# Optimization experiments

Measured on AMD Instinct MI355X. Metric: run time of the kernel, lower is better.

## Reference

```python
import jax, jax.numpy as jnp
import numpy as np
from jax import lax

B, N, C = 32, 512, 512   # N must be 8*8*8 (Convpass reshape)
H, DH = 8, 64            # heads, head_dim
ADIM = 8                 # adapter dim
MLP = 4096
EPS = 1e-5
SCALE = DH ** -0.5


def _ln(x, g, b):
    m = jnp.mean(x, axis=-1, keepdims=True)
    v = jnp.mean((x - m) ** 2, axis=-1, keepdims=True)
    return (x - m) * lax.rsqrt(v + EPS) * g + b


def _qgelu(x):
    return x * jax.nn.sigmoid(1.702 * x)


def _convpass(x, dw, db, cw, cb, uw, ub):
    # x: [B,N,C] -> down [B,N,ADIM]
    d = _qgelu(jnp.einsum('bnc,ca->bna', x, dw) + db)
    p = d.reshape(B, 8, 8, 8, ADIM).transpose(0, 4, 1, 2, 3)  # NCDHW
    p = lax.conv_general_dilated(
        p, cw, window_strides=(1, 1, 1), padding='SAME',
        dimension_numbers=('NCDHW', 'OIDHW', 'NCDHW')) + cb[None, :, None, None, None]
    p = p.transpose(0, 2, 3, 4, 1).reshape(B, N, ADIM)
    return jnp.einsum('bna,ac->bnc', _qgelu(p), uw) + ub


def _attn(x, qkv_w, proj_w, proj_b):
    qkv = jnp.einsum('bnc,ck->bnk', x, qkv_w)            # [B,N,3C]
    qkv = qkv.reshape(B, N, 3, H, DH)
    q, k, v = (qkv[:, :, i].transpose(0, 2, 1, 3) for i in range(3))  # [B,H,N,DH]
    a = jax.nn.softmax(jnp.einsum('bhnd,bhmd->bhnm', q, k) * SCALE, axis=-1)
    o = jnp.einsum('bhnm,bhmd->bhnd', a, v).transpose(0, 2, 1, 3).reshape(B, N, C)
    return jnp.einsum('bnc,ck->bnk', o, proj_w) + proj_b


def setup_inputs() -> dict:
    key = jax.random.key(0)
    ks = jax.random.split(key, 24)
    r = lambda i, shape, s=0.02: jax.random.normal(ks[i], shape, jnp.float32) * s
    inp = {
        'x': jax.random.normal(ks[0], (B, N, C), jnp.float32),
        'pos': jax.random.normal(ks[1], (B, N, C), jnp.float32),
        'ln1_g': jnp.ones((C,), jnp.float32), 'ln1_b': jnp.zeros((C,), jnp.float32),
        'qkv_w': r(2, (C, 3 * C)),
        'proj_w': r(3, (C, C)), 'proj_b': jnp.zeros((C,), jnp.float32),
        'cp1_down_w': r(4, (C, ADIM)), 'cp1_down_b': jnp.zeros((ADIM,), jnp.float32),
        'cp1_conv_w': r(5, (ADIM, ADIM, 3, 3, 3), 0.1), 'cp1_conv_b': jnp.zeros((ADIM,), jnp.float32),
        'cp1_up_w': r(6, (ADIM, C)), 'cp1_up_b': jnp.zeros((C,), jnp.float32),
        'ln2_g': jnp.ones((C,), jnp.float32), 'ln2_b': jnp.zeros((C,), jnp.float32),
        'ff_w1': r(7, (C, MLP)), 'ff_b1': jnp.zeros((MLP,), jnp.float32),
        'ff_w2': r(8, (MLP, C)), 'ff_b2': jnp.zeros((C,), jnp.float32),
        'cp2_down_w': r(9, (C, ADIM)), 'cp2_down_b': jnp.zeros((ADIM,), jnp.float32),
        'cp2_conv_w': r(10, (ADIM, ADIM, 3, 3, 3), 0.1), 'cp2_conv_b': jnp.zeros((ADIM,), jnp.float32),
        'cp2_up_w': r(11, (ADIM, C)), 'cp2_up_b': jnp.zeros((C,), jnp.float32),
    }
    return inp


def reference(x, pos, ln1_g, ln1_b, qkv_w, proj_w, proj_b,
              cp1_down_w, cp1_down_b, cp1_conv_w, cp1_conv_b, cp1_up_w, cp1_up_b,
              ln2_g, ln2_b, ff_w1, ff_b1, ff_w2, ff_b2,
              cp2_down_w, cp2_down_b, cp2_conv_w, cp2_conv_b, cp2_up_w, cp2_up_b):
    x = x + pos
    # attention stage: Residual(PreNormDrop(LN, SelfAttn, Convpass)), dropout=identity (eval)
    h = _ln(x, ln1_g, ln1_b)
    x = x + _attn(h, qkv_w, proj_w, proj_b) + _convpass(h, cp1_down_w, cp1_down_b, cp1_conv_w, cp1_conv_b, cp1_up_w, cp1_up_b)
    # FFN stage: Residual(PreNorm(LN, FFN, Convpass))
    h = _ln(x, ln2_g, ln2_b)
    ffn = jnp.einsum('bnm,mc->bnc', jax.nn.gelu(jnp.einsum('bnc,cm->bnm', h, ff_w1) + ff_b1, approximate=False), ff_w2) + ff_b2
    x = x + ffn + _convpass(h, cp2_down_w, cp2_down_b, cp2_conv_w, cp2_conv_b, cp2_up_w, cp2_up_b)
    return x
```

## Files before the change

kernel.cpp:

```cpp
#include <hip/hip_runtime.h>
#include <math.h>

typedef __bf16 bf16_t;
typedef __bf16 bf16x8 __attribute__((ext_vector_type(8)));
typedef __bf16 bf16x4 __attribute__((ext_vector_type(4)));
typedef float f32x4 __attribute__((ext_vector_type(4)));

constexpr int kB   = 32;
constexpr int kN   = 512;
constexpr int kC   = 512;
constexpr int kH   = 8;
constexpr int kAD  = 8;
constexpr int kMLP = 4096;
constexpr int kBN  = kB * kN;
constexpr float kEPS   = 1e-5f;
constexpr float kSCALE = 0.125f;

__device__ __forceinline__ float qgelu_f(float x) {
    return x / (1.f + __expf(-1.702f * x));
}
__device__ __forceinline__ float gelu_f(float x) {
    float u = 1.5957691216f * x * (1.f + 0.044715f * x * x);
    float e = __expf(u);
    float th = 1.f - 2.f / (e + 1.f);
    return 0.5f * x * (1.f + th);
}

__device__ __forceinline__ unsigned pk2(float a, float b) {
    union { bf16_t h[2]; unsigned u; } z;
    z.h[0] = (bf16_t)a; z.h[1] = (bf16_t)b;
    return z.u;
}

__device__ __forceinline__ void gld_lds16(const void* g, void* l) {
    typedef const __attribute__((address_space(1))) unsigned int* gp_t;
    typedef __attribute__((address_space(3))) unsigned int* lp_t;
    __builtin_amdgcn_global_load_lds((gp_t)(unsigned long long)g,
                                     (lp_t)(unsigned)(unsigned long long)l,
                                     16, 0, 0);
}

__global__ __launch_bounds__(256) void k_addln(
    const float* __restrict__ x, const float* __restrict__ pos,
    const float* __restrict__ g, const float* __restrict__ be,
    float* __restrict__ xout, bf16_t* __restrict__ hout,
    const float* __restrict__ cpv, const float* __restrict__ uwp,
    const float* __restrict__ ubp)
{
    int row = blockIdx.x, tid = threadIdx.x;
    size_t base = (size_t)row * kC;
    __shared__ float s8[8];
    if (cpv) {
        if (tid < 8) s8[tid] = cpv[(size_t)row * 8 + tid];
        __syncthreads();
    }
    float v0 = x[base + tid], v1 = x[base + tid + 256];
    if (pos) { v0 += pos[base + tid]; v1 += pos[base + tid + 256]; }
    if (cpv) {
        float u0 = ubp[tid], u1 = ubp[tid + 256];
        #pragma unroll
        for (int a = 0; a < 8; a++) {
            u0 += s8[a] * uwp[a * kC + tid];
            u1 += s8[a] * uwp[a * kC + tid + 256];
        }
        v0 += u0; v1 += u1;
    }
    if (xout) { xout[base + tid] = v0; xout[base + tid + 256] = v1; }
    float s = v0 + v1, q = v0 * v0 + v1 * v1;
    #pragma unroll
    for (int o = 32; o > 0; o >>= 1) {
        s += __shfl_down(s, o);
        q += __shfl_down(q, o);
    }
    __shared__ float ss[4], sq[4], mrs[2];
    int wv = tid >> 6, ln = tid & 63;
    if (!ln) { ss[wv] = s; sq[wv] = q; }
    __syncthreads();
    if (!tid) {
        float ts = ss[0] + ss[1] + ss[2] + ss[3];
        float tq = sq[0] + sq[1] + sq[2] + sq[3];
        float m = ts * (1.f / kC);
        float var = tq * (1.f / kC) - m * m;
        mrs[0] = m; mrs[1] = rsqrtf(var + kEPS);
    }
    __syncthreads();
    float m = mrs[0], r = mrs[1];
    hout[base + tid]       = (bf16_t)((v0 - m) * r * g[tid] + be[tid]);
    hout[base + tid + 256] = (bf16_t)((v1 - m) * r * g[tid + 256] + be[tid + 256]);
}

__global__ __launch_bounds__(256) void k_transpose_all(
    const float* __restrict__ qkvw, const float* __restrict__ projw,
    const float* __restrict__ fw1,  const float* __restrict__ fw2,
    bf16_t* __restrict__ qkvT, bf16_t* __restrict__ projT,
    bf16_t* __restrict__ fw1T, bf16_t* __restrict__ fw2T)
{
    int id = blockIdx.x;
    const float* w; bf16_t* wt; int K, N, bx, by;
    if (id < 768)       { w = qkvw; wt = qkvT; K = 512;  N = 1536; bx = id % 48;  by = id / 48; }
    else if (id < 1024) { id -= 768;  w = projw; wt = projT; K = 512;  N = 512;  bx = id % 16;  by = id / 16; }
    else if (id < 3072) { id -= 1024; w = fw1;   wt = fw1T;  K = 512;  N = 4096; bx = id % 128; by = id / 128; }
    else                { id -= 3072; w = fw2;   wt = fw2T;  K = 4096; N = 512;  bx = id % 16;  by = id / 16; }
    __shared__ float t[32][33];
    int n0 = bx * 32, k0 = by * 32;
    int tx = threadIdx.x & 31, ty = threadIdx.x >> 5;
    #pragma unroll
    for (int j = 0; j < 32; j += 8)
        t[ty + j][tx] = w[(size_t)(k0 + ty + j) * N + n0 + tx];
    __syncthreads();
    #pragma unroll
    for (int j = 0; j < 32; j += 8)
        wt[(size_t)(n0 + ty + j) * K + k0 + tx] = (bf16_t)t[tx][ty + j];
}

template <int ACT, bool HASB, bool HASR, int OMODE, int K, int LDA, int LDB, int NC>
__global__ __launch_bounds__(256) void k_gemm(
    const bf16_t* __restrict__ A, const bf16_t* __restrict__ Bt,
    const float* __restrict__ bias, const float* __restrict__ res,
    void* __restrict__ outv)
{
    __shared__ bf16_t As[2][128 * 32];
    __shared__ bf16_t Bs[2][128 * 32];
    int tid = threadIdx.x;
    int col0 = blockIdx.x * 128, row0 = blockIdx.y * 128;
    int w = tid >> 6, l = tid & 63;
    int rw0 = (w & 1) * 64, cw0 = (w >> 1) * 64;
    int lr = tid >> 2;
    int lc = (((tid & 3) ^ ((tid >> 3) & 3)) * 8);

    f32x4 acc[4][4];
    #pragma unroll
    for (int i = 0; i < 4; i++)
        #pragma unroll
        for (int j = 0; j < 4; j++)
            acc[i][j] = (f32x4){0.f, 0.f, 0.f, 0.f};

    const bf16_t* Ag  = A  + (size_t)(row0 + lr) * LDA + lc;
    const bf16_t* Ag2 = A  + (size_t)(row0 + 64 + lr) * LDA + lc;
    const bf16_t* Bg  = Bt + (size_t)(col0 + lr) * LDB + lc;
    const bf16_t* Bg2 = Bt + (size_t)(col0 + 64 + lr) * LDB + lc;

    int am = rw0 + (l & 15);
    int bn = cw0 + (l & 15);
    int kq = (l >> 4) * 8;
    int kqA = kq ^ (((am >> 1) & 3) << 3);
    int kqB = kq ^ (((bn >> 1) & 3) << 3);

    for (int k0 = 0; k0 < K; k0 += 64) {
        gld_lds16(Ag + k0, &As[0][tid * 8]);
        gld_lds16(Ag2 + k0, &As[0][2048 + tid * 8]);
        gld_lds16(Bg + k0, &Bs[0][tid * 8]);
        gld_lds16(Bg2 + k0, &Bs[0][2048 + tid * 8]);
        gld_lds16(Ag + k0 + 32, &As[1][tid * 8]);
        gld_lds16(Ag2 + k0 + 32, &As[1][2048 + tid * 8]);
        gld_lds16(Bg + k0 + 32, &Bs[1][tid * 8]);
        gld_lds16(Bg2 + k0 + 32, &Bs[1][2048 + tid * 8]);
        __syncthreads();
        #pragma unroll
        for (int ks = 0; ks < 2; ks++) {
            bf16x8 af[4], bfr[4];
            #pragma unroll
            for (int mt = 0; mt < 4; mt++)
                af[mt] = *(const bf16x8*)&As[ks][(am + mt * 16) * 32 + kqA];
            #pragma unroll
            for (int nt = 0; nt < 4; nt++)
                bfr[nt] = *(const bf16x8*)&Bs[ks][(bn + nt * 16) * 32 + kqB];
            #pragma unroll
            for (int mt = 0; mt < 4; mt++)
                #pragma unroll
                for (int nt = 0; nt < 4; nt++)
                    acc[mt][nt] = __builtin_amdgcn_mfma_f32_16x16x32_bf16(
                        af[mt], bfr[nt], acc[mt][nt], 0, 0, 0);
        }
        __syncthreads();
    }

    #pragma unroll
    for (int mt = 0; mt < 4; mt++) {
        int rowb = row0 + rw0 + mt * 16 + (l >> 4) * 4;
        #pragma unroll
        for (int nt = 0; nt < 4; nt++) {
            int col = col0 + cw0 + nt * 16 + (l & 15);
            float bv = HASB ? bias[col] : 0.f;
            if (OMODE == 2) {
                int which = col >> 9, hd = (col >> 6) & 7, d = col & 63;
                size_t hb = ((size_t)((rowb >> 9) * 8 + hd) * 3 + which) << 15;
                int n0 = rowb & 511;
                if (which == 2) {
                    bf16x4 pk;
                    #pragma unroll
                    for (int p = 0; p < 4; p++) pk[p] = (bf16_t)acc[mt][nt][p];
                    *(bf16x4*)((bf16_t*)outv + hb + (size_t)d * 512 + n0) = pk;
                } else {
                    #pragma unroll
                    for (int p = 0; p < 4; p++)
                        ((bf16_t*)outv)[hb + (size_t)(n0 + p) * 64 + d] =
                            (bf16_t)acc[mt][nt][p];
                }
            } else {
                #pragma unroll
                for (int p = 0; p < 4; p++) {
                    float v = acc[mt][nt][p] + bv;
                    if (ACT == 1) v = qgelu_f(v);
                    if (ACT == 2) v = gelu_f(v);
                    int r = rowb + p;
                    if (OMODE == 0) {
                        if (HASR) v += res[(size_t)r * NC + col];
                        ((float*)outv)[(size_t)r * NC + col] = v;
                    } else {
                        ((bf16_t*)outv)[(size_t)r * NC + col] = (bf16_t)v;
                    }
                }
            }
        }
    }
}

__global__ __launch_bounds__(256) void k_attn(
    const bf16_t* __restrict__ qkvb, bf16_t* __restrict__ obuf)
{
    __shared__ __align__(16) unsigned Ps[4][16 * 36];
    int bid = blockIdx.x;
    int qb = bid & 3, h = (bid >> 2) & 7, b = bid >> 5;
    int t = threadIdx.x, w = t >> 6, l = t & 63;
    const bf16_t* qp  = qkvb + (((size_t)(b * 8 + h) * 3) << 15);
    const bf16_t* kp  = qp + (1 << 15);
    const bf16_t* vtp = qp + (2 << 15);
    int q0 = qb * 128 + w * 32;
    int l15 = l & 15, g = l >> 4, lq = g * 8;
    unsigned* psw = &Ps[w][0];

    bf16x8 aq[2][2];
    #pragma unroll
    for (int mt = 0; mt < 2; mt++)
        #pragma unroll
        for (int kh = 0; kh < 2; kh++) {
            bf16x8 qv = *(const bf16x8*)(qp + (size_t)(q0 + mt * 16 + l15) * 64
                                         + kh * 32 + lq);
            #pragma unroll
            for (int e = 0; e < 8; e++) qv[e] = (bf16_t)((float)qv[e] * kSCALE);
            aq[mt][kh] = qv;
        }

    f32x4 o[2][4];
    float m_run[2], l_run[2];
    #pragma unroll
    for (int mt = 0; mt < 2; mt++) {
        m_run[mt] = -1e30f; l_run[mt] = 0.f;
        #pragma unroll
        for (int dt = 0; dt < 4; dt++) o[mt][dt] = (f32x4){0.f, 0.f, 0.f, 0.f};
    }

    for (int kt = 0; kt < 8; kt++) {
        bf16x8 kf[4][2], vf[4][2];
        #pragma unroll
        for (int nt = 0; nt < 4; nt++)
            #pragma unroll
            for (int kh = 0; kh < 2; kh++)
                kf[nt][kh] = *(const bf16x8*)(kp
                    + (size_t)(kt * 64 + nt * 16 + l15) * 64 + kh * 32 + lq);
        #pragma unroll
        for (int dt = 0; dt < 4; dt++)
            #pragma unroll
            for (int kh = 0; kh < 2; kh++)
                vf[dt][kh] = *(const bf16x8*)(vtp
                    + (size_t)(dt * 16 + l15) * 512 + kt * 64 + kh * 32 + lq);

        #pragma unroll
        for (int mt = 0; mt < 2; mt++) {
            f32x4 sc[4];
            #pragma unroll
            for (int nt = 0; nt < 4; nt++) sc[nt] = (f32x4){0.f, 0.f, 0.f, 0.f};
            #pragma unroll
            for (int nt = 0; nt < 4; nt++)
                #pragma unroll
                for (int kh = 0; kh < 2; kh++)
                    sc[nt] = __builtin_amdgcn_mfma_f32_16x16x32_bf16(
                        kf[nt][kh], aq[mt][kh], sc[nt], 0, 0, 0);
            float mx = sc[0][0];
            #pragma unroll
            for (int nt = 0; nt < 4; nt++)
                #pragma unroll
                for (int p = 0; p < 4; p++) mx = fmaxf(mx, sc[nt][p]);
            mx = fmaxf(mx, __shfl_xor(mx, 16));
            mx = fmaxf(mx, __shfl_xor(mx, 32));
            float mn = fmaxf(m_run[mt], mx);
            float alpha = __expf(m_run[mt] - mn);
            m_run[mt] = mn;
            float rs = 0.f;
            #pragma unroll
            for (int nt = 0; nt < 4; nt++)
                #pragma unroll
                for (int p = 0; p < 4; p++) {
                    float pv = __expf(sc[nt][p] - mn);
                    sc[nt][p] = pv; rs += pv;
                }
            rs += __shfl_xor(rs, 16);
            rs += __shfl_xor(rs, 32);
            l_run[mt] = l_run[mt] * alpha + rs;
            #pragma unroll
            for (int dt = 0; dt < 4; dt++)
                #pragma unroll
                for (int p = 0; p < 4; p++) o[mt][dt][p] *= alpha;
            #pragma unroll
            for (int nt = 0; nt < 4; nt++) {
                uint2 dw;
                dw.x = pk2(sc[nt][0], sc[nt][1]);
                dw.y = pk2(sc[nt][2], sc[nt][3]);
                *(uint2*)&psw[l15 * 36 + nt * 8 + g * 2] = dw;
            }
            asm volatile("" ::: "memory");
            bf16x8 pf0 = *(const bf16x8*)&psw[l15 * 36 + g * 4];
            bf16x8 pf1 = *(const bf16x8*)&psw[l15 * 36 + 16 + g * 4];
            #pragma unroll
            for (int dt = 0; dt < 4; dt++) {
                o[mt][dt] = __builtin_amdgcn_mfma_f32_16x16x32_bf16(
                    vf[dt][0], pf0, o[mt][dt], 0, 0, 0);
                o[mt][dt] = __builtin_amdgcn_mfma_f32_16x16x32_bf16(
                    vf[dt][1], pf1, o[mt][dt], 0, 0, 0);
            }
            asm volatile("" ::: "memory");
        }
    }
    #pragma unroll
    for (int mt = 0; mt < 2; mt++) {
        float inv = 1.f / l_run[mt];
        size_t rbase = ((size_t)b * 512 + q0 + mt * 16 + l15) * 512 + h * 64;
        #pragma unroll
        for (int dt = 0; dt < 4; dt++) {
            bf16x4 pk;
            #pragma unroll
            for (int p = 0; p < 4; p++) pk[p] = (bf16_t)(o[mt][dt][p] * inv);
            *(bf16x4*)&obuf[rbase + dt * 16 + g * 4] = pk;
        }
    }
}

__global__ __launch_bounds__(256) void k_down(
    const bf16_t* __restrict__ h, const float* __restrict__ dw,
    const float* __restrict__ db, float* __restrict__ outp)
{
    __shared__ float sdw[kC * kAD];
    int t = threadIdx.x;
    for (int i = t; i < kC * kAD; i += 256) sdw[i] = dw[i];
    __syncthreads();
    int gt = blockIdx.x * 256 + t;
    int row = gt >> 3, a = gt & 7;
    const bf16x8* hr = (const bf16x8*)(h + (size_t)row * kC);
    float acc = 0.f;
    for (int k8 = 0; k8 < kC / 8; k8++) {
        bf16x8 hv = hr[k8];
        #pragma unroll
        for (int e = 0; e < 8; e++)
            acc += (float)hv[e] * sdw[(k8 * 8 + e) * kAD + a];
    }
    outp[gt] = qgelu_f(acc + db[a]);
}

__global__ __launch_bounds__(512) void k_conv(
    const float* __restrict__ inp, const float* __restrict__ cw,
    const float* __restrict__ cb, float* __restrict__ outp)
{
    __shared__ float si[512 * 9];
    __shared__ float sw[8 * 8 * 27];
    int b = blockIdx.x, t = threadIdx.x;
    for (int i = t; i < 512 * 8; i += 512) {
        int n = i >> 3, a = i & 7;
        si[n * 9 + a] = inp[(size_t)b * 4096 + i];
    }
    for (int i = t; i < 1728; i += 512) sw[i] = cw[i];
    __syncthreads();
    int z = t >> 6, y = (t >> 3) & 7, xx = t & 7;
    float acc[8];
    #pragma unroll
    for (int ao = 0; ao < 8; ao++) acc[ao] = cb[ao];
    for (int dz = -1; dz <= 1; dz++) {
        int zz = z + dz; if ((unsigned)zz > 7u) continue;
        for (int dy = -1; dy <= 1; dy++) {
            int yy = y + dy; if ((unsigned)yy > 7u) continue;
            for (int dx = -1; dx <= 1; dx++) {
                int xn = xx + dx; if ((unsigned)xn > 7u) continue;
                int nn = zz * 64 + yy * 8 + xn;
                int wo = ((dz + 1) * 3 + (dy + 1)) * 3 + (dx + 1);
                #pragma unroll
                for (int ai = 0; ai < 8; ai++) {
                    float iv = si[nn * 9 + ai];
                    #pragma unroll
                    for (int ao = 0; ao < 8; ao++)
                        acc[ao] += iv * sw[(ao * 8 + ai) * 27 + wo];
                }
            }
        }
    }
    #pragma unroll
    for (int ao = 0; ao < 8; ao++)
        outp[(size_t)b * 4096 + t * 8 + ao] = qgelu_f(acc[ao]);
}

__global__ __launch_bounds__(256) void k_up(
    const float* __restrict__ pa, const float* __restrict__ uw,
    const float* __restrict__ ub, float* __restrict__ xbuf)
{
    __shared__ float s[8];
    int row = blockIdx.x, t = threadIdx.x;
    if (t < 8) s[t] = pa[(size_t)row * kAD + t];
    __syncthreads();
    #pragma unroll
    for (int rep = 0; rep < 2; rep++) {
        int c = t + rep * 256;
        float acc = ub[c];
        #pragma unroll
        for (int a = 0; a < 8; a++) acc += s[a] * uw[a * kC + c];
        xbuf[(size_t)row * kC + c] += acc;
    }
}

extern "C" void kernel_launch(void* const* d_in, const int* in_sizes, int n_in,
                              void* d_out, int out_size, void* d_ws, size_t ws_size,
                              hipStream_t stream)
{
    const float* x     = (const float*)d_in[0];
    const float* pos   = (const float*)d_in[1];
    const float* ln1g  = (const float*)d_in[2];
    const float* ln1b  = (const float*)d_in[3];
    const float* qkvw  = (const float*)d_in[4];
    const float* projw = (const float*)d_in[5];
    const float* projb = (const float*)d_in[6];
    const float* dw1   = (const float*)d_in[7];
    const float* db1   = (const float*)d_in[8];
    const float* cw1   = (const float*)d_in[9];
    const float* cb1   = (const float*)d_in[10];
    const float* uw1   = (const float*)d_in[11];
    const float* ub1   = (const float*)d_in[12];
    const float* ln2g  = (const float*)d_in[13];
    const float* ln2b  = (const float*)d_in[14];
    const float* fw1   = (const float*)d_in[15];
    const float* fb1   = (const float*)d_in[16];
    const float* fw2   = (const float*)d_in[17];
    const float* fb2   = (const float*)d_in[18];
    const float* dw2   = (const float*)d_in[19];
    const float* db2   = (const float*)d_in[20];
    const float* cw2   = (const float*)d_in[21];
    const float* cb2   = (const float*)d_in[22];
    const float* uw2   = (const float*)d_in[23];
    const float* ub2   = (const float*)d_in[24];
    float* out = (float*)d_out;

    char* wsb = (char*)d_ws;
    float*  xbuf = (float*)wsb;
    bf16_t* hb   = (bf16_t*)(wsb + 33554432);
    bf16_t* obuf = (bf16_t*)(wsb + 50331648);
    bf16_t* qkvb = (bf16_t*)(wsb + 67108864);
    bf16_t* midb = (bf16_t*)(wsb + 50331648);
    bf16_t* qkvT = (bf16_t*)(wsb + 117440512);
    bf16_t* projT= (bf16_t*)(wsb + 119013376);
    bf16_t* fw1T = (bf16_t*)(wsb + 119537664);
    bf16_t* fw2T = (bf16_t*)(wsb + 123731968);
    float*  cpa  = (float*)(wsb + 127926272);
    float*  cpb  = (float*)(wsb + 128450560);

    k_transpose_all<<<5120, 256, 0, stream>>>(
        qkvw, projw, fw1, fw2, qkvT, projT, fw1T, fw2T);

    k_addln<<<kBN, 256, 0, stream>>>(x, pos, ln1g, ln1b, xbuf, hb,
                                     nullptr, nullptr, nullptr);

    k_gemm<0, false, false, 2, 512, 512, 512, 1536>
        <<<dim3(12, 128), 256, 0, stream>>>(hb, qkvT, nullptr, nullptr, qkvb);
    k_attn<<<kB * kH * 4, 256, 0, stream>>>(qkvb, obuf);
    k_gemm<0, true, true, 0, 512, 512, 512, 512>
        <<<dim3(4, 128), 256, 0, stream>>>(obuf, projT, projb, xbuf, xbuf);

    k_down<<<kBN * kAD / 256, 256, 0, stream>>>(hb, dw1, db1, cpa);
    k_conv<<<kB, 512, 0, stream>>>(cpa, cw1, cb1, cpb);

    k_addln<<<kBN, 256, 0, stream>>>(xbuf, nullptr, ln2g, ln2b, xbuf, hb,
                                     cpb, uw1, ub1);

    k_down<<<kBN * kAD / 256, 256, 0, stream>>>(hb, dw2, db2, cpa);
    k_conv<<<kB, 512, 0, stream>>>(cpa, cw2, cb2, cpb);
    k_up<<<kBN, 256, 0, stream>>>(cpb, uw2, ub2, xbuf);

    k_gemm<2, true, false, 1, 512, 512, 512, 2048>
        <<<dim3(16, 128), 256, 0, stream>>>(hb, fw1T, fb1, nullptr, midb);
    k_gemm<0, false, true, 0, 2048, 2048, 4096, 512>
        <<<dim3(4, 128), 256, 0, stream>>>(midb, fw2T, nullptr, xbuf, xbuf);
    k_gemm<2, true, false, 1, 512, 512, 512, 2048>
        <<<dim3(16, 128), 256, 0, stream>>>(hb, fw1T + (size_t)2048 * 512,
                                            fb1 + 2048, nullptr, midb);
    k_gemm<0, true, true, 0, 2048, 2048, 4096, 512>
        <<<dim3(4, 128), 256, 0, stream>>>(midb, fw2T + 2048, fb2, xbuf, out);
}
```

Before: 637.7 us.

## Double-buffer K fragments in attention, add MFMA priority and block swizzle

The attention kernel now prefetches the next K tile into a second register buffer while computing the current one, and fully unrolls the key loop in pairs. It also raises wave priority around the MFMA sections, remaps block indices so neighbouring blocks spread across batch/head groups, and sets a minimum occupancy of 3 blocks per CU in the launch bounds. The aim is to hide global-load latency for K behind matrix work. The extra register buffer and full unrolling raise register pressure, which may force spills under the occupancy hint.

```diff
diff --git a/kernel.cpp b/kernel.cpp
--- a/kernel.cpp
+++ b/kernel.cpp
@@ -216,11 +216,12 @@
     }
 }
 
-__global__ __launch_bounds__(256) void k_attn(
+__global__ __launch_bounds__(256, 3) void k_attn(
     const bf16_t* __restrict__ qkvb, bf16_t* __restrict__ obuf)
 {
     __shared__ __align__(16) unsigned Ps[4][16 * 36];
     int bid = blockIdx.x;
+    bid = (bid & 7) * 128 + (bid >> 3);
     int qb = bid & 3, h = (bid >> 2) & 7, b = bid >> 5;
     int t = threadIdx.x, w = t >> 6, l = t & 63;
     const bf16_t* qp  = qkvb + (((size_t)(b * 8 + h) * 3) << 15);
@@ -251,32 +252,37 @@
         for (int dt = 0; dt < 4; dt++) o[mt][dt] = (f32x4){0.f, 0.f, 0.f, 0.f};
     }
 
-    for (int kt = 0; kt < 8; kt++) {
-        bf16x8 kf[4][2], vf[4][2];
-        #pragma unroll
-        for (int nt = 0; nt < 4; nt++)
-            #pragma unroll
-            for (int kh = 0; kh < 2; kh++)
-                kf[nt][kh] = *(const bf16x8*)(kp
-                    + (size_t)(kt * 64 + nt * 16 + l15) * 64 + kh * 32 + lq);
-        #pragma unroll
-        for (int dt = 0; dt < 4; dt++)
-            #pragma unroll
-            for (int kh = 0; kh < 2; kh++)
-                vf[dt][kh] = *(const bf16x8*)(vtp
-                    + (size_t)(dt * 16 + l15) * 512 + kt * 64 + kh * 32 + lq);
-
+    bf16x8 kfA[4][2], kfB[4][2], vf[4][2];
+
+#define LOADK(dst, ktv)                                                     \
+    _Pragma("unroll")                                                       \
+    for (int nt = 0; nt < 4; nt++)                                          \
+        _Pragma("unroll")                                                   \
+        for (int kh = 0; kh < 2; kh++)                                      \
+            dst[nt][kh] = *(const bf16x8*)(kp                               \
+                + (size_t)((ktv) * 64 + nt * 16 + l15) * 64 + kh * 32 + lq);
+#define LOADV(ktv)                                                          \
+    _Pragma("unroll")                                                       \
+    for (int dt = 0; dt < 4; dt++)                                          \
+        _Pragma("unroll")                                                   \
+        for (int kh = 0; kh < 2; kh++)                                      \
+            vf[dt][kh] = *(const bf16x8*)(vtp                               \
+                + (size_t)(dt * 16 + l15) * 512 + (ktv) * 64 + kh * 32 + lq);
+
+    auto body = [&](bf16x8 (&kf)[4][2]) {
         #pragma unroll
         for (int mt = 0; mt < 2; mt++) {
             f32x4 sc[4];
             #pragma unroll
             for (int nt = 0; nt < 4; nt++) sc[nt] = (f32x4){0.f, 0.f, 0.f, 0.f};
+            __builtin_amdgcn_s_setprio(1);
             #pragma unroll
             for (int nt = 0; nt < 4; nt++)
                 #pragma unroll
                 for (int kh = 0; kh < 2; kh++)
                     sc[nt] = __builtin_amdgcn_mfma_f32_16x16x32_bf16(
                         kf[nt][kh], aq[mt][kh], sc[nt], 0, 0, 0);
+            __builtin_amdgcn_s_setprio(0);
             float mx = sc[0][0];
             #pragma unroll
             for (int nt = 0; nt < 4; nt++)
@@ -312,6 +318,7 @@
             asm volatile("" ::: "memory");
             bf16x8 pf0 = *(const bf16x8*)&psw[l15 * 36 + g * 4];
             bf16x8 pf1 = *(const bf16x8*)&psw[l15 * 36 + 16 + g * 4];
+            __builtin_amdgcn_s_setprio(1);
             #pragma unroll
             for (int dt = 0; dt < 4; dt++) {
                 o[mt][dt] = __builtin_amdgcn_mfma_f32_16x16x32_bf16(
@@ -319,9 +326,25 @@
                 o[mt][dt] = __builtin_amdgcn_mfma_f32_16x16x32_bf16(
                     vf[dt][1], pf1, o[mt][dt], 0, 0, 0);
             }
+            __builtin_amdgcn_s_setprio(0);
             asm volatile("" ::: "memory");
         }
-    }
+    };
+
+    LOADK(kfA, 0);
+    #pragma unroll
+    for (int kp2 = 0; kp2 < 4; kp2++) {
+        const int kt0 = 2 * kp2;
+        LOADV(kt0);
+        LOADK(kfB, kt0 + 1);
+        body(kfA);
+        LOADV(kt0 + 1);
+        if (kp2 < 3) { LOADK(kfA, kt0 + 2); }
+        body(kfB);
+    }
+#undef LOADK
+#undef LOADV
+
     #pragma unroll
     for (int mt = 0; mt < 2; mt++) {
         float inv = 1.f / l_run[mt];
```

Result: slower. 953.5 us (+49.5%).
